# Performance work log

Hardware: AMD Instinct MI355X
Metric: run time of the kernel (lower is better)

Reference implementation:

```python
import jax, jax.numpy as jnp
import numpy as np

N_HEAD = 16
N_EMBD = 1024
B, T = 4, 1024


def setup_inputs() -> dict:
    key = jax.random.key(0)
    ks = jax.random.split(key, 8)
    hs = N_EMBD // N_HEAD
    x = jax.random.normal(ks[0], (B, T, N_EMBD), dtype=jnp.float32)
    # previous-layer attention load per token, ~O(1/T) like a softmax column mean
    refractory_state = jax.random.uniform(ks[1], (B, T), dtype=jnp.float32) / T
    s_attn = 1.0 / np.sqrt(N_EMBD)
    W_attn = jax.random.normal(ks[2], (N_EMBD, 3 * N_EMBD), dtype=jnp.float32) * s_attn
    b_attn = jnp.zeros((3 * N_EMBD,), dtype=jnp.float32)
    W_proj = jax.random.normal(ks[3], (N_EMBD, N_EMBD), dtype=jnp.float32) * s_attn
    b_proj = jnp.zeros((N_EMBD,), dtype=jnp.float32)
    # learnable LIF params, init per module (lif_mode='refractory')
    threshold = jnp.full((N_HEAD,), 0.01, dtype=jnp.float32)
    leak = jnp.full((N_HEAD,), 2.0, dtype=jnp.float32)
    steepness = jnp.full((N_HEAD,), 2.0, dtype=jnp.float32)
    ref_strength = jnp.full((N_HEAD,), -2.0, dtype=jnp.float32)
    cross_w = jnp.full((N_HEAD,), -2.0, dtype=jnp.float32)
    return {
        "x": x, "refractory_state": refractory_state,
        "W_attn": W_attn, "b_attn": b_attn,
        "W_proj": W_proj, "b_proj": b_proj,
        "threshold": threshold, "leak": leak, "steepness": steepness,
        "ref_strength": ref_strength, "cross_w": cross_w,
    }


def reference(x, refractory_state, W_attn, b_attn, W_proj, b_proj,
              threshold, leak, steepness, ref_strength, cross_w):
    Bq, Tq, C = x.shape
    H = N_HEAD
    hs = C // H
    qkv = x @ W_attn + b_attn                     # [B,T,3C]
    q, k, v = jnp.split(qkv, 3, axis=-1)
    q = q.reshape(Bq, Tq, H, hs).transpose(0, 2, 1, 3)  # [B,H,T,hs]
    k = k.reshape(Bq, Tq, H, hs).transpose(0, 2, 1, 3)
    v = v.reshape(Bq, Tq, H, hs).transpose(0, 2, 1, 3)

    att = jnp.einsum('bhqd,bhkd->bhqk', q, k) * (1.0 / jnp.sqrt(jnp.asarray(hs, x.dtype)))
    causal = jnp.tril(jnp.ones((Tq, Tq), dtype=bool))
    att = jnp.where(causal[None, None], att, -jnp.inf)
    probs = jax.nn.softmax(att, axis=-1)          # [B,H,T,T]

    thr = (jnp.abs(threshold) * 0.1)[None, :, None, None]
    lk = jax.nn.sigmoid(leak)[None, :, None, None]
    st = jax.nn.softplus(steepness)[None, :, None, None]
    # refractory: column load over queries + cross-layer load
    column_load = probs.mean(axis=-2, keepdims=True)          # [B,H,1,T]
    eff_thr = thr + jax.nn.softplus(ref_strength)[None, :, None, None] * column_load
    eff_thr = eff_thr + jax.nn.sigmoid(cross_w)[None, :, None, None] * refractory_state[:, None, None, :]

    fire = jax.nn.sigmoid(st * (probs - eff_thr))
    lif_w = fire + lk * (1.0 - fire)
    mod = probs * lif_w
    mod = mod / (mod.sum(axis=-1, keepdims=True) + 1e-8)
    new_refractory = mod.mean(axis=1).mean(axis=-2)           # [B,T]

    y = jnp.einsum('bhqk,bhkd->bhqd', mod, v)
    y = y.transpose(0, 2, 1, 3).reshape(Bq, Tq, C)
    y = y @ W_proj + b_proj
    return y, new_refractory
```

## Files before the change

kernel.cpp:

```cpp
#include <hip/hip_runtime.h>
#include <math.h>

#define B_  4
#define T_  1024
#define C_  1024
#define H_  16
#define HS_ 64
#define K2E 0.1803368801f
#define LOG2E 1.44269504f

typedef _Float16 f16;
typedef _Float16 f16x8 __attribute__((ext_vector_type(8)));
typedef float f32x4 __attribute__((ext_vector_type(4)));

#define MFMA16(a,b,c) __builtin_amdgcn_mfma_f32_16x16x32_f16(a,b,c,0,0,0)
#define EXP2(x) __builtin_amdgcn_exp2f(x)
#define RCP(x)  __builtin_amdgcn_rcpf(x)

__device__ __forceinline__ float qsum_(float v){
    v += __shfl_xor(v,1,64); v += __shfl_xor(v,2,64);
    v += __shfl_xor(v,4,64); v += __shfl_xor(v,8,64);
    return v;
}
__device__ __forceinline__ float sigmoidf_(float x){ return 1.0f/(1.0f + __expf(-x)); }
__device__ __forceinline__ float softplusf_(float x){ return fmaxf(x, 0.0f) + log1pf(__expf(-fabsf(x))); }

__global__ __launch_bounds__(256) void prep_k(
    const float* __restrict__ x, const float* __restrict__ Wa,
    const float* __restrict__ Wp,
    f16* __restrict__ x_h, f16* __restrict__ WaT, f16* __restrict__ WpT,
    float* __restrict__ zbase)
{
    __shared__ float tl[32][33];
    const int bid = blockIdx.x, tid = threadIdx.x;
    if (bid < 2048){
        int i = bid*256 + tid;
        const float4* p = (const float4*)x + (size_t)i*2;
        float4 a = p[0], b = p[1];
        f16x8 o;
        o[0]=(f16)a.x; o[1]=(f16)a.y; o[2]=(f16)a.z; o[3]=(f16)a.w;
        o[4]=(f16)b.x; o[5]=(f16)b.y; o[6]=(f16)b.z; o[7]=(f16)b.w;
        *((f16x8*)x_h + i) = o;
    } else if (bid < 5120){
        int t = bid - 2048;
        int n0 = (t % 96)*32, k0 = (t / 96)*32;
        const int c = tid & 31, r4 = tid >> 5;
        #pragma unroll
        for (int i=0;i<4;i++){ int r = r4*4+i; tl[r][c] = Wa[(size_t)(k0+r)*3072 + n0 + c]; }
        __syncthreads();
        #pragma unroll
        for (int i=0;i<4;i++){ int r = r4*4+i; WaT[(size_t)(n0+r)*1024 + k0 + c] = (f16)tl[c][r]; }
    } else if (bid < 6144){
        int t = bid - 5120;
        int n0 = (t & 31)*32, k0 = (t >> 5)*32;
        const int c = tid & 31, r4 = tid >> 5;
        #pragma unroll
        for (int i=0;i<4;i++){ int r = r4*4+i; tl[r][c] = Wp[(size_t)(k0+r)*1024 + n0 + c]; }
        __syncthreads();
        #pragma unroll
        for (int i=0;i<4;i++){ int r = r4*4+i; WpT[(size_t)(n0+r)*1024 + k0 + c] = (f16)tl[c][r]; }
    } else {
        int idx = (bid - 6144)*256 + tid;
        float4 z; z.x=0.f; z.y=0.f; z.z=0.f; z.w=0.f;
        ((float4*)zbase)[idx] = z;
    }
}

#define CT_STRIDE 132
__global__ __launch_bounds__(256) void gemm_qkv_k(
    const f16* __restrict__ A, const f16* __restrict__ Bt,
    const float* __restrict__ bias,
    f16* __restrict__ Qh, f16* __restrict__ Kh, f16* __restrict__ Vt)
{
    __shared__ __align__(16) f16 smem[16896];
    const int tid = threadIdx.x;
    const int lane = tid & 63, wave = tid >> 6;
    const int lx = lane & 15, quad = lane >> 4;
    const int wm = wave & 1, wn = wave >> 1;
    const int m0 = blockIdx.y*128, n0 = blockIdx.x*128;
    const f16* Ap = A  + (size_t)m0*1024;
    const f16* Bp = Bt + (size_t)n0*1024;
    f32x4 acc[4][4];
    #pragma unroll
    for (int i=0;i<4;i++){
        #pragma unroll
        for (int j=0;j<4;j++){ acc[i][j][0]=0.f;acc[i][j][1]=0.f;acc[i][j][2]=0.f;acc[i][j][3]=0.f; }
    }
#define GQ_LOAD(rA,rB,K0) { \
    for (int i=0;i<2;i++){ int c=i*4+wave; \
        rA[i] = *(const f16x8*)(Ap + (size_t)(c*16+lx)*1024 + (K0) + quad*8); \
        rB[i] = *(const f16x8*)(Bp + (size_t)(c*16+lx)*1024 + (K0) + quad*8); } }
#define GQ_STORE(rA,rB,BUF) { \
    for (int i=0;i<2;i++){ int c=i*4+wave; \
        *(f16x8*)&smem[(BUF) + c*512 + quad*128 + lx*8]        = rA[i]; \
        *(f16x8*)&smem[(BUF) + 4096 + c*512 + quad*128 + lx*8] = rB[i]; } }
#define GQ_COMP(BUF) { \
    f16x8 af[4], bf[4]; \
    for (int mt=0;mt<4;mt++) af[mt] = *(const f16x8*)&smem[(BUF) + (wm*4+mt)*512 + quad*128 + lx*8]; \
    for (int nt=0;nt<4;nt++) bf[nt] = *(const f16x8*)&smem[(BUF) + 4096 + (wn*4+nt)*512 + quad*128 + lx*8]; \
    for (int mt=0;mt<4;mt++) \
        for (int nt=0;nt<4;nt++) \
            acc[mt][nt] = MFMA16(af[mt], bf[nt], acc[mt][nt]); }

    f16x8 raE[2], rbE[2], raO[2], rbO[2];
    GQ_LOAD(raE, rbE, 0);
    GQ_STORE(raE, rbE, 0);
    GQ_LOAD(raO, rbO, 32);
    __syncthreads();
    #pragma unroll 1
    for (int it=0; it<32; it+=2){
        if (it+2 < 32) GQ_LOAD(raE, rbE, (it+2)*32);
        GQ_STORE(raO, rbO, 8192);
        GQ_COMP(0);
        __syncthreads();
        if (it+3 < 32) GQ_LOAD(raO, rbO, (it+3)*32);
        if (it+2 < 32) GQ_STORE(raE, rbE, 0);
        GQ_COMP(8192);
        __syncthreads();
    }
    f16* Ct = smem;
    #pragma unroll
    for (int mt=0;mt<4;mt++){
        #pragma unroll
        for (int nt=0;nt<4;nt++){
            int n_loc = wn*64 + nt*16 + lx;
            float bv = bias[n0 + n_loc];
            #pragma unroll
            for (int r=0;r<4;r++){
                int m_loc = wm*64 + mt*16 + quad*4 + r;
                Ct[m_loc*CT_STRIDE + n_loc] = (f16)(acc[mt][nt][r] + bv);
            }
        }
    }
    __syncthreads();
    const int bb = m0 >> 10;
    if (n0 < 2048){
        for (int it=0; it<8; it++){
            int row = it*32 + wave*8 + (lane>>3);
            int ch  = lane & 7;
            int m_loc = row >> 1, half = row & 1;
            f16x8 v = *(const f16x8*)&Ct[m_loc*CT_STRIDE + half*64 + ch*8];
            int n = n0 + half*64;
            int which = n >> 10, cc = n & 1023, h = cc >> 6;
            int t = (m0 + m_loc) & 1023;
            f16* dst = (which==0) ? Qh : Kh;
            *(f16x8*)(dst + ((size_t)(bb*16+h)*1024 + t)*64 + ch*8) = v;
        }
    } else {
        for (int it=0; it<8; it++){
            int drow = it*16 + wave*4 + (lane>>4);
            int ch   = lane & 15;
            int cc = (n0 + drow) & 1023;
            int h = cc >> 6, d = cc & 63;
            f16 tmp[8];
            #pragma unroll
            for (int j=0;j<8;j++) tmp[j] = Ct[(ch*8+j)*CT_STRIDE + drow];
            int t = (m0 + ch*8) & 1023;
            *(f16x8*)(Vt + ((size_t)(bb*16+h)*64 + d)*1024 + t) = *(f16x8*)tmp;
        }
    }
}

__global__ __launch_bounds__(256) void gemm_proj_k(
    const f16* __restrict__ A, const f16* __restrict__ Bt,
    const float* __restrict__ bias, float* __restrict__ out,
    const float* __restrict__ racc)
{
    if (blockIdx.x == 512){
        float* oref = out + (size_t)B_*T_*C_;
        #pragma unroll
        for (int j=0;j<16;j++){
            int idx = j*256 + threadIdx.x;
            oref[idx] = racc[idx] * (1.0f/(H_*T_));
        }
        return;
    }
    __shared__ __align__(16) f16 smem[12288];
    const int tid = threadIdx.x;
    const int lane = tid & 63, wave = tid >> 6;
    const int lx = lane & 15, quad = lane >> 4;
    const int wm = wave & 1, wn = wave >> 1;
    const int m0 = (blockIdx.x >> 4)*128, n0 = (blockIdx.x & 15)*64;
    const f16* Ap = A  + (size_t)m0*1024;
    const f16* Bp = Bt + (size_t)n0*1024;
    f32x4 acc[4][2];
    #pragma unroll
    for (int i=0;i<4;i++){
        #pragma unroll
        for (int j=0;j<2;j++){ acc[i][j][0]=0.f;acc[i][j][1]=0.f;acc[i][j][2]=0.f;acc[i][j][3]=0.f; }
    }
#define GP_LOAD(rA,rB,K0) { \
    for (int i=0;i<2;i++) \
        rA[i] = *(const f16x8*)(Ap + (size_t)((i*4+wave)*16+lx)*1024 + (K0) + quad*8); \
    rB = *(const f16x8*)(Bp + (size_t)(wave*16+lx)*1024 + (K0) + quad*8); }
#define GP_STORE(rA,rB,BUF) { \
    for (int i=0;i<2;i++) \
        *(f16x8*)&smem[(BUF) + (i*4+wave)*512 + quad*128 + lx*8] = rA[i]; \
    *(f16x8*)&smem[(BUF) + 4096 + wave*512 + quad*128 + lx*8] = rB; }
#define GP_COMP(BUF) { \
    f16x8 af[4], bf[2]; \
    for (int mt=0;mt<4;mt++) af[mt] = *(const f16x8*)&smem[(BUF) + (wm*4+mt)*512 + quad*128 + lx*8]; \
    for (int nt=0;nt<2;nt++) bf[nt] = *(const f16x8*)&smem[(BUF) + 4096 + (wn*2+nt)*512 + quad*128 + lx*8]; \
    for (int mt=0;mt<4;mt++) \
        for (int nt=0;nt<2;nt++) \
            acc[mt][nt] = MFMA16(af[mt], bf[nt], acc[mt][nt]); }

    f16x8 raE[2], raO[2], rbE, rbO;
    GP_LOAD(raE, rbE, 0);
    GP_STORE(raE, rbE, 0);
    GP_LOAD(raO, rbO, 32);
    __syncthreads();
    #pragma unroll 1
    for (int it=0; it<32; it+=2){
        if (it+2 < 32) GP_LOAD(raE, rbE, (it+2)*32);
        GP_STORE(raO, rbO, 6144);
        GP_COMP(0);
        __syncthreads();
        if (it+3 < 32) GP_LOAD(raO, rbO, (it+3)*32);
        if (it+2 < 32) GP_STORE(raE, rbE, 0);
        GP_COMP(6144);
        __syncthreads();
    }
    #pragma unroll
    for (int mt=0;mt<4;mt++){
        #pragma unroll
        for (int nt=0;nt<2;nt++){
            int n = n0 + wn*32 + nt*16 + lx;
            float bv = bias[n];
            #pragma unroll
            for (int r=0;r<4;r++){
                int m = m0 + wm*64 + mt*16 + quad*4 + r;
                out[(size_t)m*1024 + n] = acc[mt][nt][r] + bv;
            }
        }
    }
}

__global__ __launch_bounds__(256) void attn_stats_k(
    const f16* __restrict__ Qh, const f16* __restrict__ Kh,
    float* __restrict__ rowl, float* __restrict__ colp)
{
    __shared__ __align__(16) f16 Kl[8192];
    __shared__ float cacc[1024];
    const int tid = threadIdx.x;
    const int lane = tid & 63, wave = tid >> 6;
    const int lx = lane & 15, quad = lane >> 4;
    const int g  = 15 - (blockIdx.x >> 6);
    const int bh = blockIdx.x & 63;
    const int qpos = wave*16 + quad*4;
    const size_t kbase = (size_t)bh*65536;

    for (int i=tid; i<1024; i+=256) cacc[i] = 0.f;

    const size_t qoff = ((size_t)bh*1024 + g*64 + wave*16 + lx)*64;
    f16x8 aq0 = *(const f16x8*)(Qh + qoff + quad*8);
    f16x8 aq1 = *(const f16x8*)(Qh + qoff + 32 + quad*8);

#define KLOAD(dst, KT) { \
    for (int i=0;i<2;i++){ int u=i*4+wave, cc=u&3, kh=u>>2; \
        dst[i] = *(const f16x8*)(Kh + kbase + (size_t)((KT)*64 + cc*16+lx)*64 + kh*32 + quad*8); } }
#define KSTORE(src, BUF) { \
    for (int i=0;i<2;i++){ int u=i*4+wave, cc=u&3, kh=u>>2; \
        *(f16x8*)&Kl[(BUF) + cc*1024 + kh*512 + quad*128 + lx*8] = src[i]; } }
#define STATS1_TILE(KT, BUF) { \
    const bool diag = ((KT) == g); \
    for (int nt=0;nt<4;nt++){ \
        f32x4 sc = {0.f,0.f,0.f,0.f}; \
        f16x8 b0 = *(const f16x8*)&Kl[(BUF) + nt*1024 + quad*128 + lx*8]; \
        f16x8 b1 = *(const f16x8*)&Kl[(BUF) + nt*1024 + 512 + quad*128 + lx*8]; \
        sc = MFMA16(aq0, b0, sc); \
        sc = MFMA16(aq1, b1, sc); \
        for (int r=0;r<4;r++){ \
            float sv = sc[r]; \
            if (diag && (nt*16+lx) > (qpos + r)) sv = -1e4f; \
            ls[r] += EXP2(sv*K2E); \
        } } }
#define STATS2_TILE(KT, BUF) { \
    const bool diag = ((KT) == g); \
    for (int nt=0;nt<4;nt++){ \
        f32x4 sc = {0.f,0.f,0.f,0.f}; \
        f16x8 b0 = *(const f16x8*)&Kl[(BUF) + nt*1024 + quad*128 + lx*8]; \
        f16x8 b1 = *(const f16x8*)&Kl[(BUF) + nt*1024 + 512 + quad*128 + lx*8]; \
        sc = MFMA16(aq0, b0, sc); \
        sc = MFMA16(aq1, b1, sc); \
        float csum = 0.f; \
        for (int r=0;r<4;r++){ \
            float sv = sc[r]; \
            if (diag && (nt*16+lx) > (qpos + r)) sv = -1e4f; \
            csum += EXP2(sv*K2E) * invl[r]; \
        } \
        csum += __shfl_xor(csum,16,64); csum += __shfl_xor(csum,32,64); \
        if (quad == 0) atomicAdd(&cacc[(KT)*64 + nt*16 + lx], csum); } }

    f16x8 rkE[2], rkO[2];
    float ls[4] = {0.f,0.f,0.f,0.f};
    KLOAD(rkE, 0);
    KSTORE(rkE, 0);
    if (g >= 1) KLOAD(rkO, 1);
    __syncthreads();
    #pragma unroll 1
    for (int kt=0; kt<=g; kt+=2){
        if (kt+2 <= g) KLOAD(rkE, kt+2);
        if (kt+1 <= g) KSTORE(rkO, 4096);
        STATS1_TILE(kt, 0);
        __syncthreads();
        if (kt+1 <= g){
            if (kt+3 <= g) KLOAD(rkO, kt+3);
            if (kt+2 <= g) KSTORE(rkE, 0);
            STATS1_TILE(kt+1, 4096);
            __syncthreads();
        }
    }
    float invl[4];
    #pragma unroll
    for (int r=0;r<4;r++){
        float l = qsum_(ls[r]);
        if (lx == 0) rowl[(size_t)bh*1024 + g*64 + qpos + r] = l;
        invl[r] = RCP(l);
    }
    KLOAD(rkE, 0);
    KSTORE(rkE, 0);
    if (g >= 1) KLOAD(rkO, 1);
    __syncthreads();
    #pragma unroll 1
    for (int kt=0; kt<=g; kt+=2){
        if (kt+2 <= g) KLOAD(rkE, kt+2);
        if (kt+1 <= g) KSTORE(rkO, 4096);
        STATS2_TILE(kt, 0);
        __syncthreads();
        if (kt+1 <= g){
            if (kt+3 <= g) KLOAD(rkO, kt+3);
            if (kt+2 <= g) KSTORE(rkE, 0);
            STATS2_TILE(kt+1, 4096);
            __syncthreads();
        }
    }
    for (int i=tid; i<(g+1)*64; i+=256)
        atomicAdd(&colp[(size_t)bh*1024 + i], cacc[i]);
}

__global__ __launch_bounds__(256) void attn_apply_k(
    const f16* __restrict__ Qh, const f16* __restrict__ Kh, const f16* __restrict__ Vt,
    const float* __restrict__ rowl,
    const float* __restrict__ colp, const float* __restrict__ refr,
    const float* __restrict__ threshold, const float* __restrict__ leak,
    const float* __restrict__ steepness, const float* __restrict__ ref_strength,
    const float* __restrict__ cross_w,
    f16* __restrict__ Yh, float* __restrict__ racc)
{
    __shared__ __align__(16) f16 Kl[8192];
    __shared__ __align__(16) f16 Vl[8192];
    __shared__ __align__(16) f16 Pl[4][16*72];
    __shared__ float eb[1024];
    __shared__ float cacc[1024];
    const int tid = threadIdx.x;
    const int lane = tid & 63, wave = tid >> 6;
    const int lx = lane & 15, quad = lane >> 4;
    const int g  = 15 - (blockIdx.x >> 6);
    const int bh = blockIdx.x & 63;
    const int b  = bh >> 4, h = bh & 15;
    const int qpos = wave*16 + quad*4;
    const size_t kbase = (size_t)bh*65536;

    const float thr = fabsf(threshold[h])*0.1f;
    const float lk  = sigmoidf_(leak[h]);
    const float st2 = softplusf_(steepness[h]) * LOG2E;
    const float sprT= softplusf_(ref_strength[h]) * (1.0f/T_);
    const float cw  = sigmoidf_(cross_w[h]);
    const float Alk = 1.f - lk;

    {
        float4 cp = *(const float4*)(colp + (size_t)bh*1024 + tid*4);
        float4 rf = *(const float4*)(refr + (size_t)b*1024 + tid*4);
        eb[tid*4+0] = st2*(thr + sprT*cp.x + cw*rf.x);
        eb[tid*4+1] = st2*(thr + sprT*cp.y + cw*rf.y);
        eb[tid*4+2] = st2*(thr + sprT*cp.z + cw*rf.z);
        eb[tid*4+3] = st2*(thr + sprT*cp.w + cw*rf.w);
    }
    for (int i=tid; i<1024; i+=256) cacc[i] = 0.f;

    const size_t qoff = ((size_t)bh*1024 + g*64 + wave*16 + lx)*64;
    f16x8 aq0 = *(const f16x8*)(Qh + qoff + quad*8);
    f16x8 aq1 = *(const f16x8*)(Qh + qoff + 32 + quad*8);

    float invl[4];
    #pragma unroll
    for (int r=0;r<4;r++)
        invl[r] = RCP(rowl[(size_t)bh*1024 + g*64 + qpos + r]);

    f32x4 y[4];
    #pragma unroll
    for (int i=0;i<4;i++){ y[i][0]=0.f;y[i][1]=0.f;y[i][2]=0.f;y[i][3]=0.f; }
    float Dp[4] = {0.f,0.f,0.f,0.f};

#define VLOAD(dst, KT) { \
    for (int i=0;i<2;i++){ int u=i*4+wave, cc=u&3, kh=u>>2; \
        dst[i] = *(const f16x8*)(Vt + kbase + (size_t)(cc*16+lx)*1024 + (KT)*64 + kh*32 + quad*8); } }
#define VSTORE(src, BUF) { \
    for (int i=0;i<2;i++){ int u=i*4+wave, cc=u&3, kh=u>>2; \
        *(f16x8*)&Vl[(BUF) + cc*1024 + kh*512 + quad*128 + lx*8] = src[i]; } }
#define APPLY1_TILE(KT, BUF) { \
    const bool diag = ((KT) == g); \
    for (int nt=0;nt<4;nt++){ \
        f32x4 sc = {0.f,0.f,0.f,0.f}; \
        f16x8 b0 = *(const f16x8*)&Kl[(BUF) + nt*1024 + quad*128 + lx*8]; \
        f16x8 b1 = *(const f16x8*)&Kl[(BUF) + nt*1024 + 512 + quad*128 + lx*8]; \
        sc = MFMA16(aq0, b0, sc); \
        sc = MFMA16(aq1, b1, sc); \
        float ec = eb[(KT)*64 + nt*16 + lx]; \
        for (int r=0;r<4;r++){ \
            float sv = sc[r]; \
            if (diag && (nt*16+lx) > (qpos + r)) sv = -1e4f; \
            float p = EXP2(sv*K2E) * invl[r]; \
            float fire = RCP(1.f + EXP2(ec - st2*p)); \
            float pw = p * (lk + Alk*fire); \
            Dp[r] += pw; \
            Pl[wave][(quad*4+r)*72 + nt*16 + lx] = (f16)pw; \
        } } \
    { f16x8 ap0 = *(const f16x8*)&Pl[wave][lx*72 + quad*8]; \
      f16x8 ap1 = *(const f16x8*)&Pl[wave][lx*72 + 32 + quad*8]; \
      for (int dt=0;dt<4;dt++){ \
        f16x8 bv0 = *(const f16x8*)&Vl[(BUF) + dt*1024 + quad*128 + lx*8]; \
        f16x8 bv1 = *(const f16x8*)&Vl[(BUF) + dt*1024 + 512 + quad*128 + lx*8]; \
        y[dt] = MFMA16(ap0, bv0, y[dt]); \
        y[dt] = MFMA16(ap1, bv1, y[dt]); } } }
#define APPLY2_TILE(KT, BUF) { \
    const bool diag = ((KT) == g); \
    for (int nt=0;nt<4;nt++){ \
        f32x4 sc = {0.f,0.f,0.f,0.f}; \
        f16x8 b0 = *(const f16x8*)&Kl[(BUF) + nt*1024 + quad*128 + lx*8]; \
        f16x8 b1 = *(const f16x8*)&Kl[(BUF) + nt*1024 + 512 + quad*128 + lx*8]; \
        sc = MFMA16(aq0, b0, sc); \
        sc = MFMA16(aq1, b1, sc); \
        float ec = eb[(KT)*64 + nt*16 + lx]; \
        float csum = 0.f; \
        for (int r=0;r<4;r++){ \
            float sv = sc[r]; \
            if (diag && (nt*16+lx) > (qpos + r)) sv = -1e4f; \
            float p = EXP2(sv*K2E) * invl[r]; \
            float fire = RCP(1.f + EXP2(ec - st2*p)); \
            csum += p * (lk + Alk*fire) * invD[r]; \
        } \
        csum += __shfl_xor(csum,16,64); csum += __shfl_xor(csum,32,64); \
        if (quad == 0) atomicAdd(&cacc[(KT)*64 + nt*16 + lx], csum); } }

    f16x8 rkE[2], rkO[2], rvE[2], rvO[2];
    KLOAD(rkE, 0); VLOAD(rvE, 0);
    KSTORE(rkE, 0); VSTORE(rvE, 0);
    if (g >= 1){ KLOAD(rkO, 1); VLOAD(rvO, 1); }
    __syncthreads();
    #pragma unroll 1
    for (int kt=0; kt<=g; kt+=2){
        if (kt+2 <= g){ KLOAD(rkE, kt+2); VLOAD(rvE, kt+2); }
        if (kt+1 <= g){ KSTORE(rkO, 4096); VSTORE(rvO, 4096); }
        APPLY1_TILE(kt, 0);
        __syncthreads();
        if (kt+1 <= g){
            if (kt+3 <= g){ KLOAD(rkO, kt+3); VLOAD(rvO, kt+3); }
            if (kt+2 <= g){ KSTORE(rkE, 0); VSTORE(rvE, 0); }
            APPLY1_TILE(kt+1, 4096);
            __syncthreads();
        }
    }
    float invD[4];
    #pragma unroll
    for (int r=0;r<4;r++) invD[r] = RCP(qsum_(Dp[r]) + 1e-8f);
    #pragma unroll
    for (int dt=0;dt<4;dt++){
        #pragma unroll
        for (int r=0;r<4;r++)
            Pl[wave][(quad*4+r)*72 + dt*16 + lx] = (f16)(y[dt][r]*invD[r]);
    }
    #pragma unroll
    for (int it=0; it<2; it++){
        int q = it*8 + (lane>>3), ch = lane & 7;
        f16x8 v = *(const f16x8*)&Pl[wave][q*72 + ch*8];
        *(f16x8*)(Yh + (size_t)(b*1024 + g*64 + wave*16 + q)*1024 + h*64 + ch*8) = v;
    }

    KLOAD(rkE, 0);
    KSTORE(rkE, 0);
    if (g >= 1) KLOAD(rkO, 1);
    __syncthreads();
    #pragma unroll 1
    for (int kt=0; kt<=g; kt+=2){
        if (kt+2 <= g) KLOAD(rkE, kt+2);
        if (kt+1 <= g) KSTORE(rkO, 4096);
        APPLY2_TILE(kt, 0);
        __syncthreads();
        if (kt+1 <= g){
            if (kt+3 <= g) KLOAD(rkO, kt+3);
            if (kt+2 <= g) KSTORE(rkE, 0);
            APPLY2_TILE(kt+1, 4096);
            __syncthreads();
        }
    }
    for (int i=tid; i<(g+1)*64; i+=256)
        atomicAdd(&racc[(size_t)b*1024 + i], cacc[i]);
}

extern "C" void kernel_launch(void* const* d_in, const int* in_sizes, int n_in,
                              void* d_out, int out_size, void* d_ws, size_t ws_size,
                              hipStream_t stream) {
    (void)in_sizes; (void)n_in; (void)out_size; (void)ws_size;
    const float* x           = (const float*)d_in[0];
    const float* refr        = (const float*)d_in[1];
    const float* W_attn      = (const float*)d_in[2];
    const float* b_attn      = (const float*)d_in[3];
    const float* W_proj      = (const float*)d_in[4];
    const float* b_proj      = (const float*)d_in[5];
    const float* threshold   = (const float*)d_in[6];
    const float* leak        = (const float*)d_in[7];
    const float* steepness   = (const float*)d_in[8];
    const float* ref_strength= (const float*)d_in[9];
    const float* cross_w     = (const float*)d_in[10];
    float* out = (float*)d_out;

    char* ws = (char*)d_ws;
    f16* x_h = (f16*)ws;                       ws += (size_t)4096*1024*2;
    f16* WaT = (f16*)ws;                       ws += (size_t)3072*1024*2;
    f16* WpT = (f16*)ws;                       ws += (size_t)1024*1024*2;
    f16* Qh  = (f16*)ws;                       ws += (size_t)64*1024*64*2;
    f16* Kh  = (f16*)ws;                       ws += (size_t)64*1024*64*2;
    f16* Vt  = (f16*)ws;                       ws += (size_t)64*64*1024*2;
    f16* Yh  = (f16*)ws;                       ws += (size_t)4096*1024*2;
    float* rowl = (float*)ws;                  ws += (size_t)65536*4;
    float* colp = (float*)ws;                  ws += (size_t)65536*4;
    float* racc = (float*)ws;                  ws += (size_t)4096*4;

    prep_k<<<dim3(6212), dim3(256), 0, stream>>>(x, W_attn, W_proj, x_h, WaT, WpT, colp);
    gemm_qkv_k<<<dim3(24,32), dim3(256), 0, stream>>>(x_h, WaT, b_attn, Qh, Kh, Vt);
    attn_stats_k<<<dim3(1024), dim3(256), 0, stream>>>(Qh, Kh, rowl, colp);
    attn_apply_k<<<dim3(1024), dim3(256), 0, stream>>>(
        Qh, Kh, Vt, rowl, colp, refr,
        threshold, leak, steepness, ref_strength, cross_w, Yh, racc);
    gemm_proj_k<<<dim3(513), dim3(256), 0, stream>>>(Yh, WpT, b_proj, out, racc);
}
```

Baseline: 286.5 us.

## Materialize unnormalized attention probabilities in fp16 instead of recomputing QK four times

The stats kernel now writes exp(QK) tiles as fp16 to a causal-packed global buffer in its first pass. Column sums are then computed by reading that buffer back, which replaces the second QK recompute pass. The apply kernel reads P from the buffer instead of redoing QK^T, overwrites it with the modulated weights, and reuses it for the refractory column reduction. This removes three of the four QK matmul passes and the K loads, in exchange for roughly 70MB of extra global write and read traffic and fp16 rounding of the probabilities.

```diff
diff --git a/kernel.cpp b/kernel.cpp
--- a/kernel.cpp
+++ b/kernel.cpp
@@ -11,11 +11,14 @@
 
 typedef _Float16 f16;
 typedef _Float16 f16x8 __attribute__((ext_vector_type(8)));
+typedef _Float16 f16x4 __attribute__((ext_vector_type(4)));
 typedef float f32x4 __attribute__((ext_vector_type(4)));
 
 #define MFMA16(a,b,c) __builtin_amdgcn_mfma_f32_16x16x32_f16(a,b,c,0,0,0)
 #define EXP2(x) __builtin_amdgcn_exp2f(x)
 #define RCP(x)  __builtin_amdgcn_rcpf(x)
+
+#define PSTRIDE_BH 557056
 
 __device__ __forceinline__ float qsum_(float v){
     v += __shfl_xor(v,1,64); v += __shfl_xor(v,2,64);
@@ -238,10 +241,12 @@
 
 __global__ __launch_bounds__(256) void attn_stats_k(
     const f16* __restrict__ Qh, const f16* __restrict__ Kh,
-    float* __restrict__ rowl, float* __restrict__ colp)
+    float* __restrict__ rowl, float* __restrict__ colp,
+    f16* __restrict__ Pbuf)
 {
     __shared__ __align__(16) f16 Kl[8192];
-    __shared__ float cacc[1024];
+    __shared__ __align__(16) f16 Pl[4][16*72];
+    __shared__ float invl_sh[64];
     const int tid = threadIdx.x;
     const int lane = tid & 63, wave = tid >> 6;
     const int lx = lane & 15, quad = lane >> 4;
@@ -249,8 +254,8 @@
     const int bh = blockIdx.x & 63;
     const int qpos = wave*16 + quad*4;
     const size_t kbase = (size_t)bh*65536;
-
-    for (int i=tid; i<1024; i+=256) cacc[i] = 0.f;
+    const int S = (g+1)*64;
+    f16* __restrict__ Pblk = Pbuf + (size_t)bh*PSTRIDE_BH + (size_t)4096*((g*(g+1))>>1);
 
     const size_t qoff = ((size_t)bh*1024 + g*64 + wave*16 + lx)*64;
     f16x8 aq0 = *(const f16x8*)(Qh + qoff + quad*8);
@@ -273,24 +278,14 @@
         for (int r=0;r<4;r++){ \
             float sv = sc[r]; \
             if (diag && (nt*16+lx) > (qpos + r)) sv = -1e4f; \
-            ls[r] += EXP2(sv*K2E); \
-        } } }
-#define STATS2_TILE(KT, BUF) { \
-    const bool diag = ((KT) == g); \
-    for (int nt=0;nt<4;nt++){ \
-        f32x4 sc = {0.f,0.f,0.f,0.f}; \
-        f16x8 b0 = *(const f16x8*)&Kl[(BUF) + nt*1024 + quad*128 + lx*8]; \
-        f16x8 b1 = *(const f16x8*)&Kl[(BUF) + nt*1024 + 512 + quad*128 + lx*8]; \
-        sc = MFMA16(aq0, b0, sc); \
-        sc = MFMA16(aq1, b1, sc); \
-        float csum = 0.f; \
-        for (int r=0;r<4;r++){ \
-            float sv = sc[r]; \
-            if (diag && (nt*16+lx) > (qpos + r)) sv = -1e4f; \
-            csum += EXP2(sv*K2E) * invl[r]; \
-        } \
-        csum += __shfl_xor(csum,16,64); csum += __shfl_xor(csum,32,64); \
-        if (quad == 0) atomicAdd(&cacc[(KT)*64 + nt*16 + lx], csum); } }
+            float p = EXP2(sv*K2E); \
+            ls[r] += p; \
+            Pl[wave][(quad*4+r)*72 + nt*16 + lx] = (f16)p; \
+        } } \
+    for (int it2=0; it2<2; it2++){ \
+        int qq = it2*8 + (lane>>3), chh = lane & 7; \
+        f16x8 v = *(const f16x8*)&Pl[wave][qq*72 + chh*8]; \
+        *(f16x8*)(Pblk + (size_t)(wave*16+qq)*S + (KT)*64 + chh*8) = v; } }
 
     f16x8 rkE[2], rkO[2];
     float ls[4] = {0.f,0.f,0.f,0.f};
@@ -311,56 +306,57 @@
             __syncthreads();
         }
     }
-    float invl[4];
     #pragma unroll
     for (int r=0;r<4;r++){
         float l = qsum_(ls[r]);
-        if (lx == 0) rowl[(size_t)bh*1024 + g*64 + qpos + r] = l;
-        invl[r] = RCP(l);
-    }
-    KLOAD(rkE, 0);
-    KSTORE(rkE, 0);
-    if (g >= 1) KLOAD(rkO, 1);
-    __syncthreads();
-    #pragma unroll 1
-    for (int kt=0; kt<=g; kt+=2){
-        if (kt+2 <= g) KLOAD(rkE, kt+2);
-        if (kt+1 <= g) KSTORE(rkO, 4096);
-        STATS2_TILE(kt, 0);
-        __syncthreads();
-        if (kt+1 <= g){
-            if (kt+3 <= g) KLOAD(rkO, kt+3);
-            if (kt+2 <= g) KSTORE(rkE, 0);
-            STATS2_TILE(kt+1, 4096);
-            __syncthreads();
-        }
-    }
-    for (int i=tid; i<(g+1)*64; i+=256)
-        atomicAdd(&colp[(size_t)bh*1024 + i], cacc[i]);
+        if (lx == 0){
+            rowl[(size_t)bh*1024 + g*64 + qpos + r] = l;
+            invl_sh[qpos + r] = RCP(l);
+        }
+    }
+    __syncthreads();
+    if (tid < (g+1)*16){
+        const int k0 = tid*4;
+        float a0=0.f, a1=0.f, a2=0.f, a3=0.f;
+        const f16* pr = Pblk + k0;
+        #pragma unroll 4
+        for (int q=0;q<64;q++){
+            f16x4 v = *(const f16x4*)(pr + (size_t)q*S);
+            float w = invl_sh[q];
+            a0 += (float)v[0]*w; a1 += (float)v[1]*w;
+            a2 += (float)v[2]*w; a3 += (float)v[3]*w;
+        }
+        float* cp = colp + (size_t)bh*1024 + k0;
+        atomicAdd(cp+0,a0); atomicAdd(cp+1,a1);
+        atomicAdd(cp+2,a2); atomicAdd(cp+3,a3);
+    }
 }
 
 __global__ __launch_bounds__(256) void attn_apply_k(
-    const f16* __restrict__ Qh, const f16* __restrict__ Kh, const f16* __restrict__ Vt,
+    const f16* __restrict__ Vt,
     const float* __restrict__ rowl,
     const float* __restrict__ colp, const float* __restrict__ refr,
     const float* __restrict__ threshold, const float* __restrict__ leak,
     const float* __restrict__ steepness, const float* __restrict__ ref_strength,
     const float* __restrict__ cross_w,
-    f16* __restrict__ Yh, float* __restrict__ racc)
+    f16* __restrict__ Yh, float* __restrict__ racc,
+    f16* __restrict__ Pbuf)
 {
-    __shared__ __align__(16) f16 Kl[8192];
     __shared__ __align__(16) f16 Vl[8192];
     __shared__ __align__(16) f16 Pl[4][16*72];
     __shared__ float eb[1024];
-    __shared__ float cacc[1024];
+    __shared__ float invl_sh[64];
+    __shared__ float invD_sh[64];
     const int tid = threadIdx.x;
     const int lane = tid & 63, wave = tid >> 6;
     const int lx = lane & 15, quad = lane >> 4;
+    const int qr8 = lane >> 3, c8 = lane & 7;
     const int g  = 15 - (blockIdx.x >> 6);
     const int bh = blockIdx.x & 63;
     const int b  = bh >> 4, h = bh & 15;
-    const int qpos = wave*16 + quad*4;
     const size_t kbase = (size_t)bh*65536;
+    const int S = (g+1)*64;
+    f16* __restrict__ Pblk = Pbuf + (size_t)bh*PSTRIDE_BH + (size_t)4096*((g*(g+1))>>1);
 
     const float thr = fabsf(threshold[h])*0.1f;
     const float lk  = sigmoidf_(leak[h]);
@@ -377,21 +373,16 @@
         eb[tid*4+2] = st2*(thr + sprT*cp.z + cw*rf.z);
         eb[tid*4+3] = st2*(thr + sprT*cp.w + cw*rf.w);
     }
-    for (int i=tid; i<1024; i+=256) cacc[i] = 0.f;
-
-    const size_t qoff = ((size_t)bh*1024 + g*64 + wave*16 + lx)*64;
-    f16x8 aq0 = *(const f16x8*)(Qh + qoff + quad*8);
-    f16x8 aq1 = *(const f16x8*)(Qh + qoff + 32 + quad*8);
-
-    float invl[4];
-    #pragma unroll
-    for (int r=0;r<4;r++)
-        invl[r] = RCP(rowl[(size_t)bh*1024 + g*64 + qpos + r]);
+    if (tid < 64) invl_sh[tid] = RCP(rowl[(size_t)bh*1024 + g*64 + tid]);
+    __syncthreads();
+
+    const float w0 = invl_sh[wave*16 + qr8];
+    const float w1 = invl_sh[wave*16 + 8 + qr8];
 
     f32x4 y[4];
     #pragma unroll
     for (int i=0;i<4;i++){ y[i][0]=0.f;y[i][1]=0.f;y[i][2]=0.f;y[i][3]=0.f; }
-    float Dp[4] = {0.f,0.f,0.f,0.f};
+    float Dp0 = 0.f, Dp1 = 0.f;
 
 #define VLOAD(dst, KT) { \
     for (int i=0;i<2;i++){ int u=i*4+wave, cc=u&3, kh=u>>2; \
@@ -399,24 +390,28 @@
 #define VSTORE(src, BUF) { \
     for (int i=0;i<2;i++){ int u=i*4+wave, cc=u&3, kh=u>>2; \
         *(f16x8*)&Vl[(BUF) + cc*1024 + kh*512 + quad*128 + lx*8] = src[i]; } }
-#define APPLY1_TILE(KT, BUF) { \
-    const bool diag = ((KT) == g); \
-    for (int nt=0;nt<4;nt++){ \
-        f32x4 sc = {0.f,0.f,0.f,0.f}; \
-        f16x8 b0 = *(const f16x8*)&Kl[(BUF) + nt*1024 + quad*128 + lx*8]; \
-        f16x8 b1 = *(const f16x8*)&Kl[(BUF) + nt*1024 + 512 + quad*128 + lx*8]; \
-        sc = MFMA16(aq0, b0, sc); \
-        sc = MFMA16(aq1, b1, sc); \
-        float ec = eb[(KT)*64 + nt*16 + lx]; \
-        for (int r=0;r<4;r++){ \
-            float sv = sc[r]; \
-            if (diag && (nt*16+lx) > (qpos + r)) sv = -1e4f; \
-            float p = EXP2(sv*K2E) * invl[r]; \
-            float fire = RCP(1.f + EXP2(ec - st2*p)); \
-            float pw = p * (lk + Alk*fire); \
-            Dp[r] += pw; \
-            Pl[wave][(quad*4+r)*72 + nt*16 + lx] = (f16)pw; \
-        } } \
+#define PLOAD(dst, KT) { \
+    dst[0] = *(const f16x8*)(Pblk + (size_t)(wave*16 + qr8)*S + (KT)*64 + c8*8); \
+    dst[1] = *(const f16x8*)(Pblk + (size_t)(wave*16 + 8 + qr8)*S + (KT)*64 + c8*8); }
+#define APPLY1_TILE(KT, BUF, pv) { \
+    float ebv[8]; \
+    *(float4*)&ebv[0] = *(const float4*)&eb[(KT)*64 + c8*8]; \
+    *(float4*)&ebv[4] = *(const float4*)&eb[(KT)*64 + c8*8 + 4]; \
+    f16x8 o0, o1; \
+    for (int j=0;j<8;j++){ \
+        float pj = (float)pv[0][j] * w0; \
+        float fire = RCP(1.f + EXP2(ebv[j] - st2*pj)); \
+        float pw = pj*(lk + Alk*fire); \
+        Dp0 += pw; o0[j] = (f16)pw; } \
+    for (int j=0;j<8;j++){ \
+        float pj = (float)pv[1][j] * w1; \
+        float fire = RCP(1.f + EXP2(ebv[j] - st2*pj)); \
+        float pw = pj*(lk + Alk*fire); \
+        Dp1 += pw; o1[j] = (f16)pw; } \
+    *(f16x8*)&Pl[wave][qr8*72 + c8*8] = o0; \
+    *(f16x8*)&Pl[wave][(8+qr8)*72 + c8*8] = o1; \
+    *(f16x8*)(Pblk + (size_t)(wave*16 + qr8)*S + (KT)*64 + c8*8) = o0; \
+    *(f16x8*)(Pblk + (size_t)(wave*16 + 8 + qr8)*S + (KT)*64 + c8*8) = o1; \
     { f16x8 ap0 = *(const f16x8*)&Pl[wave][lx*72 + quad*8]; \
       f16x8 ap1 = *(const f16x8*)&Pl[wave][lx*72 + 32 + quad*8]; \
       for (int dt=0;dt<4;dt++){ \
@@ -424,47 +419,38 @@
         f16x8 bv1 = *(const f16x8*)&Vl[(BUF) + dt*1024 + 512 + quad*128 + lx*8]; \
         y[dt] = MFMA16(ap0, bv0, y[dt]); \
         y[dt] = MFMA16(ap1, bv1, y[dt]); } } }
-#define APPLY2_TILE(KT, BUF) { \
-    const bool diag = ((KT) == g); \
-    for (int nt=0;nt<4;nt++){ \
-        f32x4 sc = {0.f,0.f,0.f,0.f}; \
-        f16x8 b0 = *(const f16x8*)&Kl[(BUF) + nt*1024 + quad*128 + lx*8]; \
-        f16x8 b1 = *(const f16x8*)&Kl[(BUF) + nt*1024 + 512 + quad*128 + lx*8]; \
-        sc = MFMA16(aq0, b0, sc); \
-        sc = MFMA16(aq1, b1, sc); \
-        float ec = eb[(KT)*64 + nt*16 + lx]; \
-        float csum = 0.f; \
-        for (int r=0;r<4;r++){ \
-            float sv = sc[r]; \
-            if (diag && (nt*16+lx) > (qpos + r)) sv = -1e4f; \
-            float p = EXP2(sv*K2E) * invl[r]; \
-            float fire = RCP(1.f + EXP2(ec - st2*p)); \
-            csum += p * (lk + Alk*fire) * invD[r]; \
-        } \
-        csum += __shfl_xor(csum,16,64); csum += __shfl_xor(csum,32,64); \
-        if (quad == 0) atomicAdd(&cacc[(KT)*64 + nt*16 + lx], csum); } }
-
-    f16x8 rkE[2], rkO[2], rvE[2], rvO[2];
-    KLOAD(rkE, 0); VLOAD(rvE, 0);
-    KSTORE(rkE, 0); VSTORE(rvE, 0);
-    if (g >= 1){ KLOAD(rkO, 1); VLOAD(rvO, 1); }
+
+    f16x8 rvE[2], rvO[2], pvE[2], pvO[2];
+    VLOAD(rvE, 0); PLOAD(pvE, 0);
+    VSTORE(rvE, 0);
+    if (g >= 1){ VLOAD(rvO, 1); PLOAD(pvO, 1); }
     __syncthreads();
     #pragma unroll 1
     for (int kt=0; kt<=g; kt+=2){
-        if (kt+2 <= g){ KLOAD(rkE, kt+2); VLOAD(rvE, kt+2); }
-        if (kt+1 <= g){ KSTORE(rkO, 4096); VSTORE(rvO, 4096); }
-        APPLY1_TILE(kt, 0);
+        if (kt+2 <= g) VLOAD(rvE, kt+2);
+        if (kt+1 <= g) VSTORE(rvO, 4096);
+        APPLY1_TILE(kt, 0, pvE);
+        if (kt+2 <= g) PLOAD(pvE, kt+2);
         __syncthreads();
         if (kt+1 <= g){
-            if (kt+3 <= g){ KLOAD(rkO, kt+3); VLOAD(rvO, kt+3); }
-            if (kt+2 <= g){ KSTORE(rkE, 0); VSTORE(rvE, 0); }
-            APPLY1_TILE(kt+1, 4096);
+            if (kt+3 <= g) VLOAD(rvO, kt+3);
+            if (kt+2 <= g) VSTORE(rvE, 0);
+            APPLY1_TILE(kt+1, 4096, pvO);
+            if (kt+3 <= g) PLOAD(pvO, kt+3);
             __syncthreads();
         }
     }
+    Dp0 += __shfl_xor(Dp0,1,64); Dp0 += __shfl_xor(Dp0,2,64); Dp0 += __shfl_xor(Dp0,4,64);
+    Dp1 += __shfl_xor(Dp1,1,64); Dp1 += __shfl_xor(Dp1,2,64); Dp1 += __shfl_xor(Dp1,4,64);
+    if (c8 == 0){
+        invD_sh[wave*16 + qr8]     = RCP(Dp0 + 1e-8f);
+        invD_sh[wave*16 + 8 + qr8] = RCP(Dp1 + 1e-8f);
+    }
+    __syncthreads();
+
     float invD[4];
     #pragma unroll
-    for (int r=0;r<4;r++) invD[r] = RCP(qsum_(Dp[r]) + 1e-8f);
+    for (int r=0;r<4;r++) invD[r] = invD_sh[wave*16 + quad*4 + r];
     #pragma unroll
     for (int dt=0;dt<4;dt++){
         #pragma unroll
@@ -478,25 +464,21 @@
         *(f16x8*)(Yh + (size_t)(b*1024 + g*64 + wave*16 + q)*1024 + h*64 + ch*8) = v;
     }
 
-    KLOAD(rkE, 0);
-    KSTORE(rkE, 0);
-    if (g >= 1) KLOAD(rkO, 1);
-    __syncthreads();
-    #pragma unroll 1
-    for (int kt=0; kt<=g; kt+=2){
-        if (kt+2 <= g) KLOAD(rkE, kt+2);
-        if (kt+1 <= g) KSTORE(rkO, 4096);
-        APPLY2_TILE(kt, 0);
-        __syncthreads();
-        if (kt+1 <= g){
-            if (kt+3 <= g) KLOAD(rkO, kt+3);
-            if (kt+2 <= g) KSTORE(rkE, 0);
-            APPLY2_TILE(kt+1, 4096);
-            __syncthreads();
-        }
-    }
-    for (int i=tid; i<(g+1)*64; i+=256)
-        atomicAdd(&racc[(size_t)b*1024 + i], cacc[i]);
+    if (tid < (g+1)*16){
+        const int k0 = tid*4;
+        float a0=0.f, a1=0.f, a2=0.f, a3=0.f;
+        const f16* pr = Pblk + k0;
+        #pragma unroll 4
+        for (int q=0;q<64;q++){
+            f16x4 v = *(const f16x4*)(pr + (size_t)q*S);
+            float w = invD_sh[q];
+            a0 += (float)v[0]*w; a1 += (float)v[1]*w;
+            a2 += (float)v[2]*w; a3 += (float)v[3]*w;
+        }
+        float* rp = racc + (size_t)b*1024 + k0;
+        atomicAdd(rp+0,a0); atomicAdd(rp+1,a1);
+        atomicAdd(rp+2,a2); atomicAdd(rp+3,a3);
+    }
 }
 
 extern "C" void kernel_launch(void* const* d_in, const int* in_sizes, int n_in,
@@ -527,12 +509,13 @@
     float* rowl = (float*)ws;                  ws += (size_t)65536*4;
     float* colp = (float*)ws;                  ws += (size_t)65536*4;
     float* racc = (float*)ws;                  ws += (size_t)4096*4;
+    f16* Pbuf = (f16*)ws;                      ws += (size_t)64*PSTRIDE_BH*2;
 
     prep_k<<<dim3(6212), dim3(256), 0, stream>>>(x, W_attn, W_proj, x_h, WaT, WpT, colp);
     gemm_qkv_k<<<dim3(24,32), dim3(256), 0, stream>>>(x_h, WaT, b_attn, Qh, Kh, Vt);
-    attn_stats_k<<<dim3(1024), dim3(256), 0, stream>>>(Qh, Kh, rowl, colp);
+    attn_stats_k<<<dim3(1024), dim3(256), 0, stream>>>(Qh, Kh, rowl, colp, Pbuf);
     attn_apply_k<<<dim3(1024), dim3(256), 0, stream>>>(
-        Qh, Kh, Vt, rowl, colp, refr,
-        threshold, leak, steepness, ref_strength, cross_w, Yh, racc);
+        Vt, rowl, colp, refr,
+        threshold, leak, steepness, ref_strength, cross_w, Yh, racc, Pbuf);
     gemm_proj_k<<<dim3(513), dim3(256), 0, stream>>>(Yh, WpT, b_proj, out, racc);
 }
```

Result: faster. 268.2 us (-6.4%).
